# Kernel optimization log

Measured on AMD Instinct MI355X. Metric: run time of the kernel, lower is better.

## Reference

```python
import jax, jax.numpy as jnp
import numpy as np
from functools import partial

V, D, L, H, S, B, FF = 32000, 1024, 4, 16, 1024, 2, 4096
DH = D // H
PREFIX = 256
NSEG = 4
LN_EPS = 1e-5
NEG = -1e9


def _ln(x, g, b):
    m = jnp.mean(x, axis=-1, keepdims=True)
    v = jnp.mean(jnp.square(x - m), axis=-1, keepdims=True)
    return (x - m) * jax.lax.rsqrt(v + LN_EPS) * g + b


def setup_inputs() -> dict:
    key = jax.random.key(0)
    ks = jax.random.split(key, 12)
    wstd = 0.02
    inp = {}
    inp['input_ids'] = jax.random.randint(ks[0], (B, S), 0, V)
    inp['segment_ids'] = jnp.sort(jax.random.randint(ks[1], (B, S), 0, NSEG), axis=-1)
    # prefix tokens (bidirectional region): first PREFIX positions
    inp['attention_mask'] = jnp.broadcast_to(jnp.arange(S) < PREFIX, (B, S))
    inp['embedding'] = jax.random.normal(ks[2], (V, D), jnp.float32) / np.sqrt(D)
    inp['in_proj_w'] = jax.random.normal(ks[3], (L, 3 * D, D), jnp.float32) * wstd
    inp['in_proj_b'] = jnp.zeros((L, 3 * D), jnp.float32)
    inp['out_proj_w'] = jax.random.normal(ks[4], (L, D, D), jnp.float32) * wstd
    inp['out_proj_b'] = jnp.zeros((L, D), jnp.float32)
    inp['ln1_g'] = jnp.ones((L, D), jnp.float32)
    inp['ln1_b'] = jnp.zeros((L, D), jnp.float32)
    inp['ln2_g'] = jnp.ones((L, D), jnp.float32)
    inp['ln2_b'] = jnp.zeros((L, D), jnp.float32)
    inp['lin1_w'] = jax.random.normal(ks[5], (L, FF, D), jnp.float32) * wstd
    inp['lin1_b'] = jnp.zeros((L, FF), jnp.float32)
    inp['lin2_w'] = jax.random.normal(ks[6], (L, D, FF), jnp.float32) * wstd
    inp['lin2_b'] = jnp.zeros((L, D), jnp.float32)
    inp['normf_g'] = jnp.ones((D,), jnp.float32)
    inp['normf_b'] = jnp.zeros((D,), jnp.float32)
    inp['head_w'] = jax.random.normal(ks[7], (V, D), jnp.float32) / np.sqrt(D)
    inp['head_b'] = jnp.zeros((V,), jnp.float32)
    return inp


def reference(input_ids, segment_ids, attention_mask, embedding,
              in_proj_w, in_proj_b, out_proj_w, out_proj_b,
              ln1_g, ln1_b, ln2_g, ln2_b,
              lin1_w, lin1_b, lin2_w, lin2_b,
              normf_g, normf_b, head_w, head_b):
    b, s = input_ids.shape
    # combined prefix + causal + segment mask: True = allowed to attend
    causal = jnp.tril(jnp.ones((s, s), bool))                                  # (S,S)
    seg = segment_ids[:, :, None] == segment_ids[:, None, :]                   # (B,S,S)
    pref = attention_mask[:, :, None] & attention_mask[:, None, :]             # (B,S,S)
    allowed = (pref | causal[None]) & seg                                      # (B,S,S)

    x = embedding[input_ids]                                                   # (B,S,D)
    inv_sqrt_dh = 1.0 / np.sqrt(DH)

    def layer(x, p):
        wqkv, bqkv, wo, bo, g1, b1, g2, b2, w1, bb1, w2, bb2 = p
        # pre-norm self-attention (norm_first=True, dropout=0 / eval)
        h = _ln(x, g1, b1)
        qkv = h @ wqkv.T + bqkv                                                # (B,S,3D)
        q, k, v = jnp.split(qkv, 3, axis=-1)
        q = q.reshape(b, s, H, DH)
        k = k.reshape(b, s, H, DH)
        v = v.reshape(b, s, H, DH)
        scores = jnp.einsum('bqhd,bkhd->bhqk', q, k) * inv_sqrt_dh             # (B,H,S,S)
        scores = jnp.where(allowed[:, None], scores, NEG)
        a = jax.nn.softmax(scores, axis=-1)
        o = jnp.einsum('bhqk,bkhd->bqhd', a, v).reshape(b, s, D)
        x = x + o @ wo.T + bo
        # pre-norm FFN (exact-erf gelu per torch default)
        h2 = _ln(x, g2, b2)
        ff = jax.nn.gelu(h2 @ w1.T + bb1, approximate=False) @ w2.T + bb2
        return x + ff, None

    params = (in_proj_w, in_proj_b, out_proj_w, out_proj_b,
              ln1_g, ln1_b, ln2_g, ln2_b, lin1_w, lin1_b, lin2_w, lin2_b)
    x, _ = jax.lax.scan(layer, x, params)
    x = _ln(x, normf_g, normf_b)
    logits = x @ head_w.T + head_b                                             # (B,S,V)
    return logits
```

## Files before the change

### kernel.cpp

```cpp
#include <hip/hip_runtime.h>
#include <math.h>

#define S_ 1024
#define D_ 1024
#define H_ 16
#define DH_ 64
#define B_ 2
#define FF_ 4096
#define L_ 4
#define V_ 32000
#define PREFIX_ 256

using u16 = unsigned short;
typedef __attribute__((ext_vector_type(4))) u16 u16x4;
typedef __attribute__((ext_vector_type(8))) __bf16 bf16x8;
typedef __attribute__((ext_vector_type(4))) float f32x4;
typedef __attribute__((ext_vector_type(4))) float fx4;

__device__ __forceinline__ float b2f(u16 x) {
    return __uint_as_float(((unsigned)x) << 16);
}
__device__ __forceinline__ u16 f2bf(float f) {
    unsigned u = __float_as_uint(f);
    return (u16)((u + 0x7FFF + ((u >> 16) & 1)) >> 16);
}

__device__ __forceinline__ void async_lds16(const u16* g, u16* l) {
    __builtin_amdgcn_global_load_lds(
        (const __attribute__((address_space(1))) unsigned int*)g,
        (__attribute__((address_space(3))) unsigned int*)l,
        16, 0, 0);
}

template<int BM, int BN, int NWM, int NWN, int WM, int WN, int EPI>
__global__ __launch_bounds__(256)
void gemm_bt(const u16* __restrict__ A, const u16* __restrict__ Bw,
             void* __restrict__ Cout,
             const float* __restrict__ bias,
             const float* __restrict__ resid,
             const int* __restrict__ seg,
             int K, int lda, int ldb, int ldc,
             long sA, long sB, long sC)
{
    static_assert(NWM * NWN == 4, "4 waves");
    static_assert(BM == NWM * WM * 16 && BN == NWN * WN * 16, "tile");
    __shared__ __align__(16) u16 ldsA[BM * 32];
    __shared__ __align__(16) u16 ldsB[BN * 32];

    const int tid = threadIdx.x;
    const int z = blockIdx.z;

    const int nx = gridDim.x;
    int id = blockIdx.y * nx + blockIdx.x;
    const int nwg = nx * gridDim.y;
    if ((nwg & 7) == 0) {
        const int cpx = nwg >> 3;
        id = (id & 7) * cpx + (id >> 3);
    }
    const int m0 = (id / nx) * BM;
    const int n0 = (id % nx) * BN;

    const u16* Ab = A + (long)z * sA;
    const u16* Bb = Bw + (long)z * sB;

    const int lane = tid & 63;
    const int wv = tid >> 6;
    const int wm = wv / NWN;
    const int wn = wv % NWN;
    const int fr = lane & 15;
    const int fq = lane >> 4;

    f32x4 acc[WM][WN] = {};

    for (int k0 = 0; k0 < K; k0 += 32) {
        #pragma unroll
        for (int r = 0; r < BM / 64; ++r) {
            int c = tid + r * 256;
            int row = c >> 2, col = (c & 3) << 3;
            async_lds16(Ab + (long)(m0 + row) * lda + k0 + col, &ldsA[c * 8]);
        }
        #pragma unroll
        for (int r = 0; r < BN / 64; ++r) {
            int c = tid + r * 256;
            int row = c >> 2, col = (c & 3) << 3;
            async_lds16(Bb + (long)(n0 + row) * ldb + k0 + col, &ldsB[c * 8]);
        }
        __syncthreads();

        bf16x8 af[WM], bfr[WN];
        #pragma unroll
        for (int m = 0; m < WM; ++m)
            af[m] = *(const bf16x8*)&ldsA[(wm * WM * 16 + m * 16 + fr) * 32 + fq * 8];
        #pragma unroll
        for (int n = 0; n < WN; ++n)
            bfr[n] = *(const bf16x8*)&ldsB[(wn * WN * 16 + n * 16 + fr) * 32 + fq * 8];
        #pragma unroll
        for (int m = 0; m < WM; ++m)
            #pragma unroll
            for (int n = 0; n < WN; ++n)
                acc[m][n] = __builtin_amdgcn_mfma_f32_16x16x32_bf16(af[m], bfr[n], acc[m][n], 0, 0, 0);
        __syncthreads();
    }

    #pragma unroll
    for (int m = 0; m < WM; ++m) {
        const int gr0 = m0 + wm * WM * 16 + m * 16 + fq * 4;
        #pragma unroll
        for (int n = 0; n < WN; ++n) {
            const int gc = n0 + wn * WN * 16 + n * 16 + fr;
            #pragma unroll
            for (int r = 0; r < 4; ++r) {
                const int gr = gr0 + r;
                float v = acc[m][n][r];
                if (EPI == 0) {
                    ((float*)Cout)[(long)z * sC + (long)gr * ldc + gc] = v + bias[gc];
                } else if (EPI == 1) {
                    ((u16*)Cout)[(long)z * sC + (long)gr * ldc + gc] = f2bf(v + bias[gc]);
                } else if (EPI == 2) {
                    const int b = z >> 4;
                    const int sq = seg[b * S_ + gr], sk = seg[b * S_ + gc];
                    const bool allowed = (sq == sk) &&
                        ((gr >= gc) || (gr < PREFIX_ && gc < PREFIX_));
                    ((u16*)Cout)[(long)z * sC + (long)gr * ldc + gc] = f2bf(allowed ? v : -1e9f);
                } else if (EPI == 3) {
                    const int b = z >> 4, hh = z & (H_ - 1);
                    ((u16*)Cout)[((long)(b * S_ + gr)) * D_ + hh * DH_ + gc] = f2bf(v);
                } else if (EPI == 4) {
                    const long idx = (long)gr * ldc + gc;
                    ((float*)Cout)[idx] = v + bias[gc] + resid[idx];
                } else if (EPI == 5) {
                    float t = v + bias[gc];
                    float g = 0.5f * t * (1.0f + erff(t * 0.70710678118654752f));
                    ((u16*)Cout)[(long)gr * ldc + gc] = f2bf(g);
                }
            }
        }
    }
}

__global__ __launch_bounds__(256)
void ln_bf16_kernel(const float* __restrict__ x, const float* __restrict__ g,
                    const float* __restrict__ b, u16* __restrict__ out)
{
    const int row = blockIdx.x;
    const int t = threadIdx.x;
    fx4 xv = ((const fx4*)(x + (long)row * D_))[t];
    float s = xv[0] + xv[1] + xv[2] + xv[3];
    #pragma unroll
    for (int o = 32; o; o >>= 1) s += __shfl_down(s, o, 64);
    __shared__ float red[8];
    const int lane = t & 63, wv = t >> 6;
    if (lane == 0) red[wv] = s;
    __syncthreads();
    const float mean = (red[0] + red[1] + red[2] + red[3]) * (1.0f / D_);
    float d0 = xv[0] - mean, d1 = xv[1] - mean, d2 = xv[2] - mean, d3 = xv[3] - mean;
    float s2 = d0 * d0 + d1 * d1 + d2 * d2 + d3 * d3;
    #pragma unroll
    for (int o = 32; o; o >>= 1) s2 += __shfl_down(s2, o, 64);
    if (lane == 0) red[4 + wv] = s2;
    __syncthreads();
    const float var = (red[4] + red[5] + red[6] + red[7]) * (1.0f / D_);
    const float rstd = rsqrtf(var + 1e-5f);
    #pragma unroll
    for (int j = 0; j < 4; ++j) {
        const int c = t * 4 + j;
        out[(long)row * D_ + c] = f2bf((xv[j] - mean) * rstd * g[c] + b[c]);
    }
}

__global__ __launch_bounds__(256)
void softmax_kernel(u16* __restrict__ p)
{
    const long row = blockIdx.x;
    const int t = threadIdx.x;
    u16x4 raw = ((u16x4*)(p + row * S_))[t];
    float v0 = b2f(raw[0]), v1 = b2f(raw[1]), v2 = b2f(raw[2]), v3 = b2f(raw[3]);
    float mx = fmaxf(fmaxf(v0, v1), fmaxf(v2, v3));
    #pragma unroll
    for (int o = 32; o; o >>= 1) mx = fmaxf(mx, __shfl_down(mx, o, 64));
    __shared__ float red[8];
    const int lane = t & 63, wv = t >> 6;
    if (lane == 0) red[wv] = mx;
    __syncthreads();
    mx = fmaxf(fmaxf(red[0], red[1]), fmaxf(red[2], red[3]));
    v0 = expf(v0 - mx); v1 = expf(v1 - mx); v2 = expf(v2 - mx); v3 = expf(v3 - mx);
    float s = v0 + v1 + v2 + v3;
    #pragma unroll
    for (int o = 32; o; o >>= 1) s += __shfl_down(s, o, 64);
    if (lane == 0) red[4 + wv] = s;
    __syncthreads();
    const float inv = 1.0f / (red[4] + red[5] + red[6] + red[7]);
    u16x4 w;
    w[0] = f2bf(v0 * inv); w[1] = f2bf(v1 * inv);
    w[2] = f2bf(v2 * inv); w[3] = f2bf(v3 * inv);
    ((u16x4*)(p + row * S_))[t] = w;
}

__global__ __launch_bounds__(256)
void qkv_reorder_kernel(const u16* __restrict__ qkv, u16* __restrict__ q,
                        u16* __restrict__ k, u16* __restrict__ vT)
{
    const int p = blockIdx.x;
    const int b = p >> 10;
    const int s = p & (S_ - 1);
    const int t = threadIdx.x;
    const long base = (long)p * 3 * D_;
    #pragma unroll
    for (int j = 0; j < 4; ++j) {
        const int idx = t * 4 + j;
        const int hh = idx >> 6, d = idx & 63;
        u16 qv = qkv[base + idx];
        u16 kv = qkv[base + D_ + idx];
        u16 vv = qkv[base + 2 * D_ + idx];
        const long zh = (long)(b * H_ + hh);
        q[(zh * S_ + s) * DH_ + d] = f2bf(b2f(qv) * 0.125f);
        k[(zh * S_ + s) * DH_ + d] = kv;
        vT[(zh * DH_ + d) * S_ + s] = vv;
    }
}

__global__ __launch_bounds__(256)
void embed_kernel(const int* __restrict__ ids, const float* __restrict__ emb,
                  float* __restrict__ x)
{
    const int p = blockIdx.x;
    const int id = ids[p];
    ((fx4*)(x + (long)p * D_))[threadIdx.x] = ((const fx4*)(emb + (long)id * D_))[threadIdx.x];
}

__global__ __launch_bounds__(256)
void f32_to_bf16_kernel(const float* __restrict__ in, u16* __restrict__ out)
{
    const long i = ((long)blockIdx.x * 256 + threadIdx.x) * 4;
    fx4 v = *(const fx4*)(in + i);
    u16x4 o;
    o[0] = f2bf(v[0]); o[1] = f2bf(v[1]); o[2] = f2bf(v[2]); o[3] = f2bf(v[3]);
    *(u16x4*)(out + i) = o;
}

extern "C" void kernel_launch(void* const* d_in, const int* in_sizes, int n_in,
                              void* d_out, int out_size, void* d_ws, size_t ws_size,
                              hipStream_t stream)
{
    const int*   input_ids   = (const int*)d_in[0];
    const int*   segment_ids = (const int*)d_in[1];
    const float* embedding   = (const float*)d_in[3];
    const float* in_proj_w   = (const float*)d_in[4];
    const float* in_proj_b   = (const float*)d_in[5];
    const float* out_proj_w  = (const float*)d_in[6];
    const float* out_proj_b  = (const float*)d_in[7];
    const float* ln1_g       = (const float*)d_in[8];
    const float* ln1_b       = (const float*)d_in[9];
    const float* ln2_g       = (const float*)d_in[10];
    const float* ln2_b       = (const float*)d_in[11];
    const float* lin1_w      = (const float*)d_in[12];
    const float* lin1_b      = (const float*)d_in[13];
    const float* lin2_w      = (const float*)d_in[14];
    const float* lin2_b      = (const float*)d_in[15];
    const float* normf_g     = (const float*)d_in[16];
    const float* normf_b     = (const float*)d_in[17];
    const float* head_w      = (const float*)d_in[18];
    const float* head_b      = (const float*)d_in[19];
    float* out = (float*)d_out;

    char* wp = (char*)d_ws;
    auto alloc = [&](size_t n) { char* p = wp; wp += (n + 255) & ~(size_t)255; return p; };
    u16* wqkv = (u16*)alloc((size_t)L_ * 3 * D_ * D_ * 2);
    u16* wo   = (u16*)alloc((size_t)L_ * D_ * D_ * 2);
    u16* w1   = (u16*)alloc((size_t)L_ * FF_ * D_ * 2);
    u16* w2   = (u16*)alloc((size_t)L_ * D_ * FF_ * 2);
    u16* wh   = (u16*)alloc((size_t)V_ * D_ * 2);
    float* x  = (float*)alloc((size_t)B_ * S_ * D_ * 4);
    u16* h    = (u16*)alloc((size_t)B_ * S_ * D_ * 2);
    u16* qkv  = (u16*)alloc((size_t)B_ * S_ * 3 * D_ * 2);
    u16* q    = (u16*)alloc((size_t)B_ * H_ * S_ * DH_ * 2);
    u16* k    = (u16*)alloc((size_t)B_ * H_ * S_ * DH_ * 2);
    u16* vT   = (u16*)alloc((size_t)B_ * H_ * S_ * DH_ * 2);
    u16* sc   = (u16*)alloc((size_t)B_ * H_ * S_ * S_ * 2);
    u16* o    = (u16*)alloc((size_t)B_ * S_ * D_ * 2);
    u16* ff   = (u16*)alloc((size_t)B_ * S_ * FF_ * 2);

    f32_to_bf16_kernel<<<L_ * 3 * D_ * D_ / 1024, 256, 0, stream>>>(in_proj_w, wqkv);
    f32_to_bf16_kernel<<<L_ * D_ * D_ / 1024, 256, 0, stream>>>(out_proj_w, wo);
    f32_to_bf16_kernel<<<L_ * FF_ * D_ / 1024, 256, 0, stream>>>(lin1_w, w1);
    f32_to_bf16_kernel<<<L_ * D_ * FF_ / 1024, 256, 0, stream>>>(lin2_w, w2);
    f32_to_bf16_kernel<<<V_ * D_ / 1024, 256, 0, stream>>>(head_w, wh);

    embed_kernel<<<B_ * S_, 256, 0, stream>>>(input_ids, embedding, x);

    for (int l = 0; l < L_; ++l) {
        ln_bf16_kernel<<<B_ * S_, 256, 0, stream>>>(x, ln1_g + l * D_, ln1_b + l * D_, h);
        gemm_bt<128, 128, 2, 2, 4, 4, 1><<<dim3(3 * D_ / 128, B_ * S_ / 128, 1), 256, 0, stream>>>(
            h, wqkv + (long)l * 3 * D_ * D_, qkv, in_proj_b + l * 3 * D_, nullptr, nullptr,
            D_, D_, D_, 3 * D_, 0, 0, 0);
        qkv_reorder_kernel<<<B_ * S_, 256, 0, stream>>>(qkv, q, k, vT);
        gemm_bt<128, 128, 2, 2, 4, 4, 2><<<dim3(S_ / 128, S_ / 128, B_ * H_), 256, 0, stream>>>(
            q, k, sc, nullptr, nullptr, segment_ids,
            DH_, DH_, DH_, S_, (long)S_ * DH_, (long)S_ * DH_, (long)S_ * S_);
        softmax_kernel<<<B_ * H_ * S_, 256, 0, stream>>>(sc);
        gemm_bt<64, 64, 2, 2, 2, 2, 3><<<dim3(1, S_ / 64, B_ * H_), 256, 0, stream>>>(
            sc, vT, o, nullptr, nullptr, nullptr,
            S_, S_, S_, 0, (long)S_ * S_, (long)DH_ * S_, 0);
        gemm_bt<64, 128, 2, 2, 2, 4, 4><<<dim3(D_ / 128, B_ * S_ / 64, 1), 256, 0, stream>>>(
            o, wo + (long)l * D_ * D_, x, out_proj_b + l * D_, x, nullptr,
            D_, D_, D_, D_, 0, 0, 0);
        ln_bf16_kernel<<<B_ * S_, 256, 0, stream>>>(x, ln2_g + l * D_, ln2_b + l * D_, h);
        gemm_bt<128, 128, 2, 2, 4, 4, 5><<<dim3(FF_ / 128, B_ * S_ / 128, 1), 256, 0, stream>>>(
            h, w1 + (long)l * FF_ * D_, ff, lin1_b + l * FF_, nullptr, nullptr,
            D_, D_, D_, FF_, 0, 0, 0);
        gemm_bt<64, 128, 2, 2, 2, 4, 4><<<dim3(D_ / 128, B_ * S_ / 64, 1), 256, 0, stream>>>(
            ff, w2 + (long)l * D_ * FF_, x, lin2_b + l * D_, x, nullptr,
            FF_, FF_, FF_, D_, 0, 0, 0);
    }

    ln_bf16_kernel<<<B_ * S_, 256, 0, stream>>>(x, normf_g, normf_b, h);
    gemm_bt<128, 128, 2, 2, 4, 4, 0><<<dim3(V_ / 128, B_ * S_ / 128, 1), 256, 0, stream>>>(
        h, wh, out, head_b, nullptr, nullptr,
        D_, D_, D_, V_, 0, 0, 0);
}
```

Baseline: 1.453 ms.

## Add 256x256 tiled 8-wave GEMM with async LDS pipelining for FFN1 and head

Introduces a new gemm256 kernel with 256x256 block tiles, 8 waves, a BK=64 double-buffered async global-to-LDS pipeline, XOR-swizzled LDS layout, interleaved MFMA and staging with setprio, and an XCD-aware block remap. It replaces the 128x128 gemm_bt for the FFN up-projection (with GELU epilogue) and the vocabulary head projection, the two largest GEMMs. The aim is higher arithmetic intensity and better latency hiding. It uses 128KB of dynamic shared memory per block and assumes dimensions divisible by 256.

```diff
diff --git a/kernel.cpp b/kernel.cpp
--- a/kernel.cpp
+++ b/kernel.cpp
@@ -32,6 +32,142 @@
         16, 0, 0);
 }
 
+template<int EPI>
+__global__ __launch_bounds__(512, 2)
+void gemm256(const u16* __restrict__ A, const u16* __restrict__ Bw,
+             void* __restrict__ Cout, const float* __restrict__ bias,
+             int K, int lda, int ldb, int ldc)
+{
+    extern __shared__ u16 lds[];
+    const int tid = threadIdx.x;
+    const int lane = tid & 63;
+    const int wv = tid >> 6;
+    const int wm = wv >> 2;
+    const int wn = wv & 3;
+    const int fr = lane & 15;
+    const int fq = lane >> 4;
+
+    const int nx = gridDim.x;
+    int id = blockIdx.y * nx + blockIdx.x;
+    const int nwg = nx * gridDim.y;
+    if ((nwg & 7) == 0) { const int cpx = nwg >> 3; id = (id & 7) * cpx + (id >> 3); }
+    const int m0 = (id / nx) * 256;
+    const int n0 = (id % nx) * 256;
+
+    const int r_in = lane >> 3;
+    const int c_sw = ((lane & 7) ^ r_in) * 8;
+    const u16* sA0 = A  + (size_t)(m0 + wv * 16 +     r_in) * lda + c_sw;
+    const u16* sA1 = A  + (size_t)(m0 + wv * 16 + 8 + r_in) * lda + c_sw;
+    const u16* sB0 = Bw + (size_t)(n0 + wv * 16 +     r_in) * ldb + c_sw;
+    const u16* sB1 = Bw + (size_t)(n0 + wv * 16 + 8 + r_in) * ldb + c_sw;
+
+    auto stageA = [&](int b, int h, int k0) {
+        u16* d = lds + b * 16384 + h * 8192 + wv * 1024;
+        async_lds16(sA0 + (size_t)h * 128 * lda + k0, d);
+        async_lds16(sA1 + (size_t)h * 128 * lda + k0, d + 512);
+    };
+    auto stageB = [&](int b, int h, int k0) {
+        u16* d = lds + 32768 + b * 16384 + h * 8192 + wv * 1024;
+        async_lds16(sB0 + (size_t)h * 128 * ldb + k0, d);
+        async_lds16(sB1 + (size_t)h * 128 * ldb + k0, d + 512);
+    };
+    auto readA = [&](int b, int h, int m, int ks) -> bf16x8 {
+        const int r = wm * 64 + m * 16 + fr;
+        const int col = (ks * 32 + fq * 8) ^ ((fr & 7) << 3);
+        return *(const bf16x8*)&lds[b * 16384 + h * 8192 + r * 64 + col];
+    };
+    auto readB = [&](int b, int h, int n, int ks) -> bf16x8 {
+        const int r = wn * 32 + n * 16 + fr;
+        const int col = (ks * 32 + fq * 8) ^ ((fr & 7) << 3);
+        return *(const bf16x8*)&lds[32768 + b * 16384 + h * 8192 + r * 64 + col];
+    };
+
+    f32x4 acc[2][2][4][2] = {};
+    bf16x8 a[4][2], b0[2][2], b1[2][2];
+
+#define VMW(n) asm volatile("s_waitcnt vmcnt(" #n ")" ::: "memory")
+#define BAR() do { __builtin_amdgcn_sched_barrier(0); __builtin_amdgcn_s_barrier(); \
+                   __builtin_amdgcn_sched_barrier(0); } while (0)
+#define MFMA16(h, j, bb) do { \
+    __builtin_amdgcn_s_setprio(1); \
+    _Pragma("unroll") for (int m = 0; m < 4; ++m) \
+    _Pragma("unroll") for (int n = 0; n < 2; ++n) \
+    _Pragma("unroll") for (int ks = 0; ks < 2; ++ks) \
+        acc[h][j][m][n] = __builtin_amdgcn_mfma_f32_16x16x32_bf16(a[m][ks], bb[n][ks], acc[h][j][m][n], 0, 0, 0); \
+    __builtin_amdgcn_s_setprio(0); } while (0)
+
+    const int NT = K >> 6;
+    stageA(0, 0, 0); stageB(0, 0, 0); stageB(0, 1, 0); stageA(0, 1, 0);
+
+    for (int t = 0; t < NT - 1; ++t) {
+        const int cur = t & 1, nxt = cur ^ 1, k1 = (t + 1) << 6;
+        VMW(4); BAR();
+        #pragma unroll
+        for (int m = 0; m < 4; ++m) { a[m][0] = readA(cur, 0, m, 0); a[m][1] = readA(cur, 0, m, 1); }
+        #pragma unroll
+        for (int n = 0; n < 2; ++n) { b0[n][0] = readB(cur, 0, n, 0); b0[n][1] = readB(cur, 0, n, 1); }
+        stageA(nxt, 0, k1);
+        MFMA16(0, 0, b0);
+        VMW(4); BAR();
+        #pragma unroll
+        for (int n = 0; n < 2; ++n) { b1[n][0] = readB(cur, 1, n, 0); b1[n][1] = readB(cur, 1, n, 1); }
+        stageB(nxt, 0, k1);
+        MFMA16(0, 1, b1);
+        VMW(4); BAR();
+        #pragma unroll
+        for (int m = 0; m < 4; ++m) { a[m][0] = readA(cur, 1, m, 0); a[m][1] = readA(cur, 1, m, 1); }
+        stageB(nxt, 1, k1);
+        MFMA16(1, 0, b0);
+        VMW(4); BAR();
+        stageA(nxt, 1, k1);
+        MFMA16(1, 1, b1);
+    }
+    {
+        const int cur = (NT - 1) & 1;
+        VMW(4); BAR();
+        #pragma unroll
+        for (int m = 0; m < 4; ++m) { a[m][0] = readA(cur, 0, m, 0); a[m][1] = readA(cur, 0, m, 1); }
+        #pragma unroll
+        for (int n = 0; n < 2; ++n) { b0[n][0] = readB(cur, 0, n, 0); b0[n][1] = readB(cur, 0, n, 1); }
+        MFMA16(0, 0, b0);
+        VMW(2); BAR();
+        #pragma unroll
+        for (int n = 0; n < 2; ++n) { b1[n][0] = readB(cur, 1, n, 0); b1[n][1] = readB(cur, 1, n, 1); }
+        MFMA16(0, 1, b1);
+        VMW(0); BAR();
+        #pragma unroll
+        for (int m = 0; m < 4; ++m) { a[m][0] = readA(cur, 1, m, 0); a[m][1] = readA(cur, 1, m, 1); }
+        MFMA16(1, 0, b0);
+        MFMA16(1, 1, b1);
+    }
+#undef VMW
+#undef BAR
+#undef MFMA16
+
+    #pragma unroll
+    for (int h = 0; h < 2; ++h)
+    #pragma unroll
+    for (int j = 0; j < 2; ++j)
+    #pragma unroll
+    for (int m = 0; m < 4; ++m)
+    #pragma unroll
+    for (int n = 0; n < 2; ++n) {
+        const int gr0 = m0 + h * 128 + wm * 64 + m * 16 + fq * 4;
+        const int gc  = n0 + j * 128 + wn * 32 + n * 16 + fr;
+        #pragma unroll
+        for (int r = 0; r < 4; ++r) {
+            const float v = acc[h][j][m][n][r];
+            if (EPI == 0) {
+                ((float*)Cout)[(size_t)(gr0 + r) * ldc + gc] = v + bias[gc];
+            } else if (EPI == 5) {
+                const float tt = v + bias[gc];
+                const float g = 0.5f * tt * (1.0f + erff(tt * 0.70710678118654752f));
+                ((u16*)Cout)[(size_t)(gr0 + r) * ldc + gc] = f2bf(g);
+            }
+        }
+    }
+}
+
 template<int BM, int BN, int NWM, int NWN, int WM, int WN, int EPI>
 __global__ __launch_bounds__(256)
 void gemm_bt(const u16* __restrict__ A, const u16* __restrict__ Bw,
@@ -112,9 +248,7 @@
             for (int r = 0; r < 4; ++r) {
                 const int gr = gr0 + r;
                 float v = acc[m][n][r];
-                if (EPI == 0) {
-                    ((float*)Cout)[(long)z * sC + (long)gr * ldc + gc] = v + bias[gc];
-                } else if (EPI == 1) {
+                if (EPI == 1) {
                     ((u16*)Cout)[(long)z * sC + (long)gr * ldc + gc] = f2bf(v + bias[gc]);
                 } else if (EPI == 2) {
                     const int b = z >> 4;
@@ -128,10 +262,6 @@
                 } else if (EPI == 4) {
                     const long idx = (long)gr * ldc + gc;
                     ((float*)Cout)[idx] = v + bias[gc] + resid[idx];
-                } else if (EPI == 5) {
-                    float t = v + bias[gc];
-                    float g = 0.5f * t * (1.0f + erff(t * 0.70710678118654752f));
-                    ((u16*)Cout)[(long)gr * ldc + gc] = f2bf(g);
                 }
             }
         }
@@ -263,6 +393,11 @@
     const float* head_b      = (const float*)d_in[19];
     float* out = (float*)d_out;
 
+    (void)hipFuncSetAttribute((const void*)&gemm256<0>,
+        hipFuncAttributeMaxDynamicSharedMemorySize, 131072);
+    (void)hipFuncSetAttribute((const void*)&gemm256<5>,
+        hipFuncAttributeMaxDynamicSharedMemorySize, 131072);
+
     char* wp = (char*)d_ws;
     auto alloc = [&](size_t n) { char* p = wp; wp += (n + 255) & ~(size_t)255; return p; };
     u16* wqkv = (u16*)alloc((size_t)L_ * 3 * D_ * D_ * 2);
@@ -305,16 +440,14 @@
             o, wo + (long)l * D_ * D_, x, out_proj_b + l * D_, x, nullptr,
             D_, D_, D_, D_, 0, 0, 0);
         ln_bf16_kernel<<<B_ * S_, 256, 0, stream>>>(x, ln2_g + l * D_, ln2_b + l * D_, h);
-        gemm_bt<128, 128, 2, 2, 4, 4, 5><<<dim3(FF_ / 128, B_ * S_ / 128, 1), 256, 0, stream>>>(
-            h, w1 + (long)l * FF_ * D_, ff, lin1_b + l * FF_, nullptr, nullptr,
-            D_, D_, D_, FF_, 0, 0, 0);
+        gemm256<5><<<dim3(FF_ / 256, B_ * S_ / 256), 512, 131072, stream>>>(
+            h, w1 + (long)l * FF_ * D_, ff, lin1_b + l * FF_, D_, D_, D_, FF_);
         gemm_bt<64, 128, 2, 2, 2, 4, 4><<<dim3(D_ / 128, B_ * S_ / 64, 1), 256, 0, stream>>>(
             ff, w2 + (long)l * D_ * FF_, x, lin2_b + l * D_, x, nullptr,
             FF_, FF_, FF_, D_, 0, 0, 0);
     }
 
     ln_bf16_kernel<<<B_ * S_, 256, 0, stream>>>(x, normf_g, normf_b, h);
-    gemm_bt<128, 128, 2, 2, 4, 4, 0><<<dim3(V_ / 128, B_ * S_ / 128, 1), 256, 0, stream>>>(
-        h, wh, out, head_b, nullptr, nullptr,
-        D_, D_, D_, V_, 0, 0, 0);
-}
+    gemm256<0><<<dim3(V_ / 256, B_ * S_ / 256), 512, 131072, stream>>>(
+        h, wh, out, head_b, D_, D_, D_, V_);
+}
```

Result: faster. 1.400 ms (-3.6%).
